# Optimization experiments

Hardware: AMD Instinct MI355X
Metric: run time of the kernel (lower is better)

The kernel has to match this reference:

```python
import jax, jax.numpy as jnp
import numpy as np

NUM_EXPERTS = 8
TOP_K = 2


def setup_inputs() -> dict:
    key = jax.random.key(0)
    ks = jax.random.split(key, 8)
    B, S, D, H, E = 4, 2048, 1024, 2048, NUM_EXPERTS
    sd = 1.0 / np.sqrt(D)
    sh = 1.0 / np.sqrt(H)
    return {
        "x": jax.random.normal(ks[0], (B, S, D), dtype=jnp.float32),
        "noise": jax.random.normal(ks[1], (B, S, E), dtype=jnp.float32),
        "router_w": jax.random.normal(ks[2], (E, D), dtype=jnp.float32) * sd,
        "router_b": jnp.zeros((E,), dtype=jnp.float32),
        "noise_w": jax.random.normal(ks[3], (E, D), dtype=jnp.float32) * sd,
        "noise_b": jnp.zeros((E,), dtype=jnp.float32),
        "w1": jax.random.normal(ks[4], (E, H, D), dtype=jnp.float32) * sd,
        "w2": jax.random.normal(ks[5], (E, D, H), dtype=jnp.float32) * sh,
        "w3": jax.random.normal(ks[6], (E, H, D), dtype=jnp.float32) * sd,
    }


def reference(x, noise, router_w, router_b, noise_w, noise_b, w1, w2, w3):
    B, S, D = x.shape
    T = B * S
    xf = x.reshape(T, D)                                  # [T, D]
    noise_f = noise.reshape(T, -1)                        # [T, E]

    # Noisy top-k router
    logits = xf @ router_w.T + router_b                   # [T, E]
    noise_logits = xf @ noise_w.T + noise_b               # [T, E]
    noisy = logits + noise_f * jax.nn.softplus(noise_logits)
    top_vals, top_idx = jax.lax.top_k(noisy, TOP_K)       # [T, K]
    sparse = jnp.full_like(noisy, -jnp.inf)
    sparse = sparse.at[jnp.arange(T)[:, None], top_idx].set(top_vals)
    gates = jax.nn.softmax(sparse, axis=-1)               # [T, E]; zero off top-k

    # Expert SwiGLU combine. Gates are exactly 0 for non-selected experts, so
    # the masked gather/scatter loop of the original equals this weighted sum.
    out = jnp.zeros_like(xf)
    for i in range(NUM_EXPERTS):
        h = jax.nn.silu(xf @ w1[i].T) * (xf @ w3[i].T)    # [T, H]
        out = out + gates[:, i:i + 1] * (h @ w2[i].T)     # [T, D]
    return out.reshape(B, S, D)
```

## Files before the change

### kernel.cpp

```cpp
#include <hip/hip_runtime.h>

typedef unsigned short u16;
typedef __attribute__((ext_vector_type(8))) __bf16 bf16x8;
typedef __attribute__((ext_vector_type(8))) short short8;
typedef __attribute__((ext_vector_type(4))) float f32x4;

#define NE 8

#define SBAR()      asm volatile("s_barrier" ::: "memory")
#define WAIT_LGKM0() do { asm volatile("s_waitcnt lgkmcnt(0)" ::: "memory"); \
                          __builtin_amdgcn_sched_barrier(0); } while (0)
#define WAIT_VM6()  asm volatile("s_waitcnt vmcnt(6)" ::: "memory")
#define WAIT_VM8()  asm volatile("s_waitcnt vmcnt(8)" ::: "memory")

__device__ __forceinline__ u16 f2bf(float f) {
    union { float f; unsigned u; } v; v.f = f;
    unsigned u = v.u;
    return (u16)((u + 0x7fffu + ((u >> 16) & 1u)) >> 16);
}

__device__ __forceinline__ f32x4 mfma16(short8 a, short8 b, f32x4 c) {
    return __builtin_amdgcn_mfma_f32_16x16x32_bf16(
        __builtin_bit_cast(bf16x8, a), __builtin_bit_cast(bf16x8, b), c, 0, 0, 0);
}

__device__ __forceinline__ void gl2lds(const u16* g, u16* l) {
    __builtin_amdgcn_global_load_lds((const __attribute__((address_space(1))) void*)g,
                                     (__attribute__((address_space(3))) void*)l,
                                     16, 0, 0);
}

__global__ void cvt_kernel(const float* __restrict__ in, u16* __restrict__ out, size_t n4) {
    size_t i = (size_t)blockIdx.x * blockDim.x + threadIdx.x;
    size_t stride = (size_t)gridDim.x * blockDim.x;
    for (; i < n4; i += stride) {
        float4 v = ((const float4*)in)[i];
        ushort4 o;
        o.x = f2bf(v.x); o.y = f2bf(v.y); o.z = f2bf(v.z); o.w = f2bf(v.w);
        ((ushort4*)out)[i] = o;
    }
}

__global__ void cvt_w13_kernel(const float* __restrict__ w1, const float* __restrict__ w3,
                               u16* __restrict__ wc, int H, int D) {
    size_t n = (size_t)NE * H * (D / 4);
    size_t i = (size_t)blockIdx.x * blockDim.x + threadIdx.x;
    size_t stride = (size_t)gridDim.x * blockDim.x;
    int d4n = D / 4;
    for (; i < n; i += stride) {
        int d4 = (int)(i % d4n);
        size_t rem = i / d4n;
        int j = (int)(rem % H);
        int e = (int)(rem / H);
        float4 v1 = ((const float4*)w1)[i];
        float4 v3 = ((const float4*)w3)[i];
        ushort4 o1, o3;
        o1.x = f2bf(v1.x); o1.y = f2bf(v1.y); o1.z = f2bf(v1.z); o1.w = f2bf(v1.w);
        o3.x = f2bf(v3.x); o3.y = f2bf(v3.y); o3.z = f2bf(v3.z); o3.w = f2bf(v3.w);
        int wcrow = ((j >> 4) << 5) + (j & 15);
        size_t o = (((size_t)e * 2 * H + wcrow) * d4n + d4);
        ((ushort4*)wc)[o] = o1;
        ((ushort4*)wc)[o + (size_t)16 * d4n] = o3;
    }
}

__global__ void router_kernel(const float* __restrict__ x, const float* __restrict__ noise,
                              const float* __restrict__ rw, const float* __restrict__ rb,
                              const float* __restrict__ nw, const float* __restrict__ nb,
                              int* __restrict__ tops, float* __restrict__ gpair,
                              u16* __restrict__ xb, int T, int D) {
    int wv = threadIdx.x >> 6;
    int lane = threadIdx.x & 63;
    int t = blockIdx.x * 4 + wv;
    if (t >= T) return;

    const float4* x4 = (const float4*)(x + (size_t)t * D) + lane * 4;
    float4 xv0 = x4[0], xv1 = x4[1], xv2 = x4[2], xv3 = x4[3];

    {
        ushort4 s0, s1, s2, s3;
        s0.x = f2bf(xv0.x); s0.y = f2bf(xv0.y); s0.z = f2bf(xv0.z); s0.w = f2bf(xv0.w);
        s1.x = f2bf(xv1.x); s1.y = f2bf(xv1.y); s1.z = f2bf(xv1.z); s1.w = f2bf(xv1.w);
        s2.x = f2bf(xv2.x); s2.y = f2bf(xv2.y); s2.z = f2bf(xv2.z); s2.w = f2bf(xv2.w);
        s3.x = f2bf(xv3.x); s3.y = f2bf(xv3.y); s3.z = f2bf(xv3.z); s3.w = f2bf(xv3.w);
        ushort4* o = (ushort4*)(xb + (size_t)t * D + lane * 16);
        o[0] = s0; o[1] = s1; o[2] = s2; o[3] = s3;
    }

    float acc[2 * NE];
#pragma unroll
    for (int e = 0; e < NE; e++) {
        const float4* w4 = (const float4*)(rw + (size_t)e * D) + lane * 4;
        float4 a = w4[0], b = w4[1], c = w4[2], d = w4[3];
        acc[e] = xv0.x*a.x + xv0.y*a.y + xv0.z*a.z + xv0.w*a.w
               + xv1.x*b.x + xv1.y*b.y + xv1.z*b.z + xv1.w*b.w
               + xv2.x*c.x + xv2.y*c.y + xv2.z*c.z + xv2.w*c.w
               + xv3.x*d.x + xv3.y*d.y + xv3.z*d.z + xv3.w*d.w;
        const float4* v4 = (const float4*)(nw + (size_t)e * D) + lane * 4;
        a = v4[0]; b = v4[1]; c = v4[2]; d = v4[3];
        acc[NE + e] = xv0.x*a.x + xv0.y*a.y + xv0.z*a.z + xv0.w*a.w
                    + xv1.x*b.x + xv1.y*b.y + xv1.z*b.z + xv1.w*b.w
                    + xv2.x*c.x + xv2.y*c.y + xv2.z*c.z + xv2.w*c.w
                    + xv3.x*d.x + xv3.y*d.y + xv3.z*d.z + xv3.w*d.w;
    }
#pragma unroll
    for (int m = 1; m < 64; m <<= 1) {
#pragma unroll
        for (int k = 0; k < 2 * NE; k++) acc[k] += __shfl_xor(acc[k], m);
    }

    if (lane == 0) {
        float v0 = -1e30f, v1 = -1e30f;
        int i0 = 0, i1 = 0;
#pragma unroll
        for (int e = 0; e < NE; e++) {
            float z = acc[NE + e] + nb[e];
            float sp = (z > 20.f) ? z : log1pf(expf(z));
            float nv = acc[e] + rb[e] + noise[(size_t)t * NE + e] * sp;
            if (nv > v0) { v1 = v0; i1 = i0; v0 = nv; i0 = e; }
            else if (nv > v1) { v1 = nv; i1 = e; }
        }
        float e1 = expf(v1 - v0);
        float inv = 1.f / (1.f + e1);
        tops[t] = i0 | (i1 << 8);
        gpair[2 * t]     = inv;
        gpair[2 * t + 1] = e1 * inv;
    }
}

__global__ void build_kernel(const int* __restrict__ tops, const float* __restrict__ gpair,
                             int* __restrict__ counts, int* __restrict__ list,
                             float* __restrict__ glist, int* __restrict__ tokslot, int T) {
    int e = blockIdx.x;
    int tid = threadIdx.x, lane = tid & 63, wv = tid >> 6;
    __shared__ int wsum[4];
    __shared__ int sbase;
    if (tid == 0) sbase = 0;
    __syncthreads();
    for (int t0 = 0; t0 < T; t0 += 256) {
        int t = t0 + tid;
        int pk = tops[t];
        int i0 = pk & 0xff, i1 = (pk >> 8) & 0xff;
        bool f0 = (i0 == e), f1 = (i1 == e);
        bool f = f0 || f1;
        unsigned long long m = __ballot(f);
        int lpos = __popcll(m & (((unsigned long long)1 << lane) - 1ull));
        if (lane == 0) wsum[wv] = __popcll(m);
        __syncthreads();
        int woff = sbase;
        for (int w = 0; w < wv; w++) woff += wsum[w];
        int tot = wsum[0] + wsum[1] + wsum[2] + wsum[3];
        if (f) {
            int pos = woff + lpos;
            list[e * T + pos]  = t;
            glist[e * T + pos] = f0 ? gpair[2 * t] : gpair[2 * t + 1];
            tokslot[2 * t + (f0 ? 0 : 1)] = (e << 16) | pos;
        }
        __syncthreads();
        if (tid == 0) sbase += tot;
    }
    __syncthreads();
    if (tid == 0) counts[e] = sbase;
}

__global__ void scan_kernel(const int* __restrict__ counts, int* __restrict__ offsets,
                            int* __restrict__ bmap, int* __restrict__ nb) {
    if (threadIdx.x == 0 && blockIdx.x == 0) {
        int s = 0, t = 0;
        for (int e = 0; e < NE; e++) {
            offsets[e] = s;
            int c = counts[e];
            s += c;
            int m = (c + 255) >> 8;
            for (int i = 0; i < m; i++) bmap[t++] = (e << 16) | i;
        }
        offsets[NE] = s;
        nb[0] = t;
    }
}


#define PH_RD_A(B, MQ) { \
    _Pragma("unroll") for (int m4 = 0; m4 < 4; m4++) { \
        aF[m4][0] = *(const short8*)&lds[B][0][(MQ)*8192 + aRow + m4*1024 + cA0]; \
        aF[m4][1] = *(const short8*)&lds[B][0][(MQ)*8192 + aRow + m4*1024 + cA1]; } }

#define PH_RD_B(B, NQ) { \
    _Pragma("unroll") for (int n2 = 0; n2 < 2; n2++) { \
        bF[n2][0] = *(const short8*)&lds[B][1][(NQ)*8192 + bRow + n2*1024 + cA0]; \
        bF[n2][1] = *(const short8*)&lds[B][1][(NQ)*8192 + bRow + n2*1024 + cA1]; } }

#define PH_MMA(MQ, NQ) do { \
    __builtin_amdgcn_s_setprio(1); \
    _Pragma("unroll") for (int m4 = 0; m4 < 4; m4++) \
        _Pragma("unroll") for (int n2 = 0; n2 < 2; n2++) { \
            acc[(MQ)*4+m4][(NQ)*2+n2] = mfma16(aF[m4][0], bF[n2][0], acc[(MQ)*4+m4][(NQ)*2+n2]); \
            acc[(MQ)*4+m4][(NQ)*2+n2] = mfma16(aF[m4][1], bF[n2][1], acc[(MQ)*4+m4][(NQ)*2+n2]); } \
    __builtin_amdgcn_s_setprio(0); } while (0)

#define STAGE(B, AB, H, p0, p1) do { \
    u16* d_ = &lds[B][AB][(H)*8192 + wid*512]; \
    gl2lds(p0, d_); gl2lds(p1, d_ + 4096); \
    p0 += 64; p1 += 64; } while (0)

#define G_TILE(B, u, nt) do { \
     \
    PH_RD_A(B, 0); PH_RD_B(B, 0); \
    if ((u) + 1 < (nt)) STAGE((B)^1, 0, 1, pA10, pA11); \
    SBAR(); WAIT_LGKM0(); \
    PH_MMA(0, 0); \
    WAIT_VM6(); \
    SBAR(); \
     \
    PH_RD_B(B, 1); \
    if ((u) + 1 < (nt)) STAGE((B)^1, 1, 1, pB10, pB11); \
    SBAR(); WAIT_LGKM0(); \
    PH_MMA(0, 1); \
    SBAR(); \
     \
    PH_RD_A(B, 1); PH_RD_B(B, 0); \
    if ((u) + 2 < (nt)) STAGE(B, 0, 0, pA00, pA01); \
    SBAR(); WAIT_LGKM0(); \
    PH_MMA(1, 0); \
    SBAR(); \
     \
    PH_RD_B(B, 1); \
    if ((u) + 2 < (nt)) STAGE(B, 1, 0, pB00, pB01); \
    SBAR(); WAIT_LGKM0(); \
    PH_MMA(1, 1); \
    WAIT_VM8(); \
    SBAR(); } while (0)

__launch_bounds__(512, 2)
__global__ void gemm1_kernel(const u16* __restrict__ xb, const u16* __restrict__ wc,
                             const int* __restrict__ counts, const int* __restrict__ offsets,
                             const int* __restrict__ list, const float* __restrict__ glist,
                             const int* __restrict__ bmap, const int* __restrict__ nb,
                             u16* __restrict__ hb, int T, int D, int H) {
    if ((int)blockIdx.y >= nb[0]) return;
    int info = bmap[blockIdx.y];
    int e = info >> 16, mblk = info & 0xffff, nblk = blockIdx.x;
    int count = counts[e];

    __shared__ u16 lds[2][2][16384];
    __shared__ int stok[256];
    __shared__ float sgate[256];

    int tid = threadIdx.x;
    int lane = tid & 63, wid = tid >> 6;

    if (tid < 256) {
        int rr = min(mblk * 256 + tid, count - 1);
        stok[tid]  = list[e * T + rr];
        sgate[tid] = glist[e * T + rr];
    }
    __syncthreads();

    const u16* wcp = wc + ((size_t)e * 2 * H + (size_t)nblk * 256) * D;

    int row_local = tid >> 3, c8 = tid & 7;
    int c_glob = c8 ^ (row_local & 7);
    const u16* pA00 = xb + (size_t)stok[row_local] * D + c_glob * 8;
    const u16* pA01 = xb + (size_t)stok[64 + row_local] * D + c_glob * 8;
    const u16* pA10 = xb + (size_t)stok[128 + row_local] * D + c_glob * 8;
    const u16* pA11 = xb + (size_t)stok[192 + row_local] * D + c_glob * 8;
    const u16* pB00 = wcp + (size_t)row_local * D + c_glob * 8;
    const u16* pB01 = wcp + (size_t)(64 + row_local) * D + c_glob * 8;
    const u16* pB10 = wcp + (size_t)(128 + row_local) * D + c_glob * 8;
    const u16* pB11 = wcp + (size_t)(192 + row_local) * D + c_glob * 8;

    int r = lane & 15, q = lane >> 4;
    int swz = r & 7;
    int cA0 = (q ^ swz) * 8;
    int cA1 = ((q + 4) ^ swz) * 8;
    int wr = wid >> 2, wc4 = wid & 3;
    int aRow = (wr * 64 + r) * 64;
    int bRow = (wc4 * 32 + r) * 64;

    f32x4 acc[8][4];
#pragma unroll
    for (int mi = 0; mi < 8; mi++)
#pragma unroll
        for (int ni = 0; ni < 4; ni++) acc[mi][ni] = (f32x4)0.f;

    short8 aF[4][2], bF[2][2];

    STAGE(0, 0, 0, pA00, pA01);
    STAGE(0, 0, 1, pA10, pA11);
    STAGE(0, 1, 0, pB00, pB01);
    STAGE(0, 1, 1, pB10, pB11);
    STAGE(1, 0, 0, pA00, pA01);
    STAGE(1, 1, 0, pB00, pB01);
    WAIT_VM6();
    SBAR();

    const int nt = D >> 6;
    for (int u = 0; u < nt; u += 2) {
        G_TILE(0, u, nt);
        G_TILE(1, u + 1, nt);
    }

    int hrow0 = offsets[e];
#pragma unroll
    for (int mi = 0; mi < 8; mi++) {
        int lrow0 = (mi >> 2) * 128 + wr * 64 + (mi & 3) * 16 + q * 4;
#pragma unroll
        for (int a = 0; a < 2; a++) {
            int col = nblk * 128 + a * 64 + wc4 * 16 + r;
#pragma unroll
            for (int tt = 0; tt < 4; tt++) {
                int lrow = lrow0 + tt;
                int grow = mblk * 256 + lrow;
                if (grow < count) {
                    float v = acc[mi][2 * a][tt];
                    float hv = v / (1.f + expf(-v)) * acc[mi][2 * a + 1][tt] * sgate[lrow];
                    hb[(size_t)(hrow0 + grow) * H + col] = f2bf(hv);
                }
            }
        }
    }
}

__launch_bounds__(512, 2)
__global__ void gemm2_kernel(const u16* __restrict__ hb, const u16* __restrict__ w2b,
                             const int* __restrict__ counts, const int* __restrict__ offsets,
                             const int* __restrict__ bmap, const int* __restrict__ nb,
                             float* __restrict__ o2, int T, int D, int H) {
    if ((int)blockIdx.y >= nb[0]) return;
    int info = bmap[blockIdx.y];
    int e = info >> 16, mblk = info & 0xffff, nblk = blockIdx.x;
    int count = counts[e];

    __shared__ u16 lds[2][2][16384];

    int tid = threadIdx.x;
    int lane = tid & 63, wid = tid >> 6;
    int off0 = offsets[e];
    const u16* w2p = w2b + ((size_t)e * D + (size_t)nblk * 256) * H;

    int row_local = tid >> 3, c8 = tid & 7;
    int c_glob = c8 ^ (row_local & 7);
    int ra00 = min(mblk * 256 + row_local, count - 1);
    int ra01 = min(mblk * 256 + 64 + row_local, count - 1);
    int ra10 = min(mblk * 256 + 128 + row_local, count - 1);
    int ra11 = min(mblk * 256 + 192 + row_local, count - 1);
    const u16* pA00 = hb + (size_t)(off0 + ra00) * H + c_glob * 8;
    const u16* pA01 = hb + (size_t)(off0 + ra01) * H + c_glob * 8;
    const u16* pA10 = hb + (size_t)(off0 + ra10) * H + c_glob * 8;
    const u16* pA11 = hb + (size_t)(off0 + ra11) * H + c_glob * 8;
    const u16* pB00 = w2p + (size_t)row_local * H + c_glob * 8;
    const u16* pB01 = w2p + (size_t)(64 + row_local) * H + c_glob * 8;
    const u16* pB10 = w2p + (size_t)(128 + row_local) * H + c_glob * 8;
    const u16* pB11 = w2p + (size_t)(192 + row_local) * H + c_glob * 8;

    int r = lane & 15, q = lane >> 4;
    int swz = r & 7;
    int cA0 = (q ^ swz) * 8;
    int cA1 = ((q + 4) ^ swz) * 8;
    int wr = wid >> 2, wc4 = wid & 3;
    int aRow = (wr * 64 + r) * 64;
    int bRow = (wc4 * 32 + r) * 64;

    f32x4 acc[8][4];
#pragma unroll
    for (int mi = 0; mi < 8; mi++)
#pragma unroll
        for (int ni = 0; ni < 4; ni++) acc[mi][ni] = (f32x4)0.f;

    short8 aF[4][2], bF[2][2];

    STAGE(0, 0, 0, pA00, pA01);
    STAGE(0, 0, 1, pA10, pA11);
    STAGE(0, 1, 0, pB00, pB01);
    STAGE(0, 1, 1, pB10, pB11);
    STAGE(1, 0, 0, pA00, pA01);
    STAGE(1, 1, 0, pB00, pB01);
    WAIT_VM6();
    SBAR();

    const int nt = H >> 6;
    for (int u = 0; u < nt; u += 2) {
        G_TILE(0, u, nt);
        G_TILE(1, u + 1, nt);
    }

#pragma unroll
    for (int mi = 0; mi < 8; mi++) {
        int lrow0 = (mi >> 2) * 128 + wr * 64 + (mi & 3) * 16 + q * 4;
#pragma unroll
        for (int tt = 0; tt < 4; tt++) {
            int grow = mblk * 256 + lrow0 + tt;
            if (grow < count) {
#pragma unroll
                for (int ni = 0; ni < 4; ni++) {
                    int col = nblk * 256 + (ni >> 1) * 128 + wc4 * 32 + (ni & 1) * 16 + r;
                    o2[(size_t)(off0 + grow) * D + col] = acc[mi][ni][tt];
                }
            }
        }
    }
}

__global__ void combine_kernel(const float* __restrict__ o2, const int* __restrict__ tokslot,
                               const int* __restrict__ offsets, float* __restrict__ out, int D) {
    int t = blockIdx.x;
    int s0 = tokslot[2 * t], s1 = tokslot[2 * t + 1];
    size_t r0 = offsets[s0 >> 16] + (s0 & 0xffff);
    size_t r1 = offsets[s1 >> 16] + (s1 & 0xffff);
    int c = threadIdx.x * 4;
    float4 a = *(const float4*)(o2 + r0 * D + c);
    float4 b = *(const float4*)(o2 + r1 * D + c);
    float4 o; o.x = a.x + b.x; o.y = a.y + b.y; o.z = a.z + b.z; o.w = a.w + b.w;
    *(float4*)(out + (size_t)t * D + c) = o;
}

extern "C" void kernel_launch(void* const* d_in, const int* in_sizes, int n_in,
                              void* d_out, int out_size, void* d_ws, size_t ws_size,
                              hipStream_t stream) {
    const float* x     = (const float*)d_in[0];
    const float* noise = (const float*)d_in[1];
    const float* rw    = (const float*)d_in[2];
    const float* rb    = (const float*)d_in[3];
    const float* nw    = (const float*)d_in[4];
    const float* nb_   = (const float*)d_in[5];
    const float* w1    = (const float*)d_in[6];
    const float* w2    = (const float*)d_in[7];
    const float* w3    = (const float*)d_in[8];
    float* out = (float*)d_out;

    const int E = NE;
    const int D = in_sizes[2] / E;
    const int T = in_sizes[0] / D;
    const int H = in_sizes[6] / (E * D);

    auto al = [](size_t v) { return (v + 255) & ~(size_t)255; };
    char* p = (char*)d_ws;
    size_t o_counts  = 0;
    size_t o_offsets = 64;
    size_t o_nb      = 128;
    size_t o_bmap    = 256;
    size_t o_tslot   = al(o_bmap  + 2048);
    size_t o_list    = al(o_tslot + (size_t)2 * T * 4);
    size_t o_glist   = al(o_list  + (size_t)E * T * 4);
    size_t o_xb      = al(o_glist + (size_t)E * T * 4);
    size_t o_wc      = al(o_xb    + (size_t)T * D * 2);
    size_t o_w2b     = al(o_wc    + (size_t)E * 2 * H * D * 2);
    size_t o_hb      = al(o_w2b   + (size_t)E * D * H * 2);

    int*   counts  = (int*)(p + o_counts);
    int*   offsets = (int*)(p + o_offsets);
    int*   nblk    = (int*)(p + o_nb);
    int*   bmap    = (int*)(p + o_bmap);
    int*   tokslot = (int*)(p + o_tslot);
    int*   list    = (int*)(p + o_list);
    float* glist   = (float*)(p + o_glist);
    u16*   xb      = (u16*)(p + o_xb);
    u16*   wc      = (u16*)(p + o_wc);
    float* o2      = (float*)(p + o_wc);
    u16*   w2b     = (u16*)(p + o_w2b);
    u16*   hb      = (u16*)(p + o_hb);
    int*   tops    = (int*)(p + o_hb);
    float* gpair   = (float*)(p + o_hb + (size_t)T * 4);

    cvt_w13_kernel<<<2048, 256, 0, stream>>>(w1, w3, wc, H, D);
    cvt_kernel<<<2048, 256, 0, stream>>>(w2, w2b, (size_t)E * D * H / 4);

    router_kernel<<<(T + 3) / 4, 256, 0, stream>>>(x, noise, rw, rb, nw, nb_,
                                                   tops, gpair, xb, T, D);
    build_kernel<<<NE, 256, 0, stream>>>(tops, gpair, counts, list, glist, tokslot, T);
    scan_kernel<<<1, 64, 0, stream>>>(counts, offsets, bmap, nblk);

    int maxb = 2 * T / 256 + NE;
    dim3 g1(2 * H / 256, maxb, 1);
    gemm1_kernel<<<g1, 512, 0, stream>>>(xb, wc, counts, offsets, list, glist,
                                         bmap, nblk, hb, T, D, H);
    dim3 g2(D / 256, maxb, 1);
    gemm2_kernel<<<g2, 512, 0, stream>>>(hb, w2b, counts, offsets,
                                         bmap, nblk, o2, T, D, H);
    combine_kernel<<<T, 256, 0, stream>>>(o2, tokslot, offsets, out, D);
}
```

Measured before the change: 625.1 us.

## Restructure GEMM main loop to hold both B fragments and reorder MFMA phases

Rewrites the shared GEMM tile macro used by both expert GEMMs. B fragments for both column halves now sit in registers, so each tile does fewer LDS read phases and barriers, and the MMA order (00, 01, 11, 10) reuses the loaded fragments. The explicit lgkmcnt waits are removed in favour of compiler-inserted ones. Global-to-LDS staging is reordered so both B halves of the next-next tile are issued together, the prologue prefetches one more stage, and the vmcnt thresholds change, with a full drain on the last tiles. This costs more registers per thread, and the changed barrier placement risks LDS races if the hazards are not fully covered.

```diff
diff --git a/kernel.cpp b/kernel.cpp
--- a/kernel.cpp
+++ b/kernel.cpp
@@ -7,11 +7,10 @@
 
 #define NE 8
 
-#define SBAR()      asm volatile("s_barrier" ::: "memory")
-#define WAIT_LGKM0() do { asm volatile("s_waitcnt lgkmcnt(0)" ::: "memory"); \
-                          __builtin_amdgcn_sched_barrier(0); } while (0)
-#define WAIT_VM6()  asm volatile("s_waitcnt vmcnt(6)" ::: "memory")
-#define WAIT_VM8()  asm volatile("s_waitcnt vmcnt(8)" ::: "memory")
+#define SBAR()   asm volatile("s_barrier" ::: "memory")
+#define WVM0()   asm volatile("s_waitcnt vmcnt(0)" ::: "memory")
+#define WVM8()   asm volatile("s_waitcnt vmcnt(8)" ::: "memory")
+#define WVM10()  asm volatile("s_waitcnt vmcnt(10)" ::: "memory")
 
 __device__ __forceinline__ u16 f2bf(float f) {
     union { float f; unsigned u; } v; v.f = f;
@@ -180,55 +179,60 @@
 }
 
 
-#define PH_RD_A(B, MQ) { \
+#define RD_A(BUF, MQ) { \
     _Pragma("unroll") for (int m4 = 0; m4 < 4; m4++) { \
-        aF[m4][0] = *(const short8*)&lds[B][0][(MQ)*8192 + aRow + m4*1024 + cA0]; \
-        aF[m4][1] = *(const short8*)&lds[B][0][(MQ)*8192 + aRow + m4*1024 + cA1]; } }
-
-#define PH_RD_B(B, NQ) { \
+        aX[m4][0] = *(const short8*)&lds[BUF][0][(MQ)*8192 + aRow + m4*1024 + cA0]; \
+        aX[m4][1] = *(const short8*)&lds[BUF][0][(MQ)*8192 + aRow + m4*1024 + cA1]; } }
+
+#define RD_B(BUF, NQ, BR) { \
     _Pragma("unroll") for (int n2 = 0; n2 < 2; n2++) { \
-        bF[n2][0] = *(const short8*)&lds[B][1][(NQ)*8192 + bRow + n2*1024 + cA0]; \
-        bF[n2][1] = *(const short8*)&lds[B][1][(NQ)*8192 + bRow + n2*1024 + cA1]; } }
-
-#define PH_MMA(MQ, NQ) do { \
+        BR[n2][0] = *(const short8*)&lds[BUF][1][(NQ)*8192 + bRow + n2*1024 + cA0]; \
+        BR[n2][1] = *(const short8*)&lds[BUF][1][(NQ)*8192 + bRow + n2*1024 + cA1]; } }
+
+#define MMA(MQ, NQ, BR) do { \
     __builtin_amdgcn_s_setprio(1); \
     _Pragma("unroll") for (int m4 = 0; m4 < 4; m4++) \
         _Pragma("unroll") for (int n2 = 0; n2 < 2; n2++) { \
-            acc[(MQ)*4+m4][(NQ)*2+n2] = mfma16(aF[m4][0], bF[n2][0], acc[(MQ)*4+m4][(NQ)*2+n2]); \
-            acc[(MQ)*4+m4][(NQ)*2+n2] = mfma16(aF[m4][1], bF[n2][1], acc[(MQ)*4+m4][(NQ)*2+n2]); } \
+            acc[(MQ)*4+m4][(NQ)*2+n2] = mfma16(aX[m4][0], BR[n2][0], acc[(MQ)*4+m4][(NQ)*2+n2]); \
+            acc[(MQ)*4+m4][(NQ)*2+n2] = mfma16(aX[m4][1], BR[n2][1], acc[(MQ)*4+m4][(NQ)*2+n2]); } \
     __builtin_amdgcn_s_setprio(0); } while (0)
 
-#define STAGE(B, AB, H, p0, p1) do { \
-    u16* d_ = &lds[B][AB][(H)*8192 + wid*512]; \
+#define STAGE(BUF, AB, HF, p0, p1) do { \
+    u16* d_ = &lds[BUF][AB][(HF)*8192 + wid*512]; \
     gl2lds(p0, d_); gl2lds(p1, d_ + 4096); \
     p0 += 64; p1 += 64; } while (0)
 
-#define G_TILE(B, u, nt) do { \
+#define TILE(BUF, t, nt) do { \
+    bool tail = (t) >= (nt) - 2; \
      \
-    PH_RD_A(B, 0); PH_RD_B(B, 0); \
-    if ((u) + 1 < (nt)) STAGE((B)^1, 0, 1, pA10, pA11); \
-    SBAR(); WAIT_LGKM0(); \
-    PH_MMA(0, 0); \
-    WAIT_VM6(); \
+    if ((t) + 1 < (nt)) STAGE(BUF ^ 1, 0, 1, pA10, pA11); \
+    RD_A(BUF, 0); RD_B(BUF, 0, bX); RD_B(BUF, 1, bY); \
+    MMA(0, 0, bX); \
     SBAR(); \
      \
-    PH_RD_B(B, 1); \
-    if ((u) + 1 < (nt)) STAGE((B)^1, 1, 1, pB10, pB11); \
-    SBAR(); WAIT_LGKM0(); \
-    PH_MMA(0, 1); \
+    if ((t) + 2 < (nt)) STAGE(BUF, 0, 0, pA00, pA01); \
+    MMA(0, 1, bY); \
+    if (tail) { WVM0(); } else { WVM10(); } \
     SBAR(); \
      \
-    PH_RD_A(B, 1); PH_RD_B(B, 0); \
-    if ((u) + 2 < (nt)) STAGE(B, 0, 0, pA00, pA01); \
-    SBAR(); WAIT_LGKM0(); \
-    PH_MMA(1, 0); \
+    if ((t) + 2 < (nt)) { STAGE(BUF, 1, 0, pB00, pB01); STAGE(BUF, 1, 1, pB10, pB11); } \
+    RD_A(BUF, 1); \
+    MMA(1, 1, bY); \
     SBAR(); \
      \
-    PH_RD_B(B, 1); \
-    if ((u) + 2 < (nt)) STAGE(B, 1, 0, pB00, pB01); \
-    SBAR(); WAIT_LGKM0(); \
-    PH_MMA(1, 1); \
-    WAIT_VM8(); \
+    MMA(1, 0, bX); \
+    if (tail) { WVM0(); } else { WVM8(); } \
+    SBAR(); } while (0)
+
+#define GEMM_PROLOGUE() do { \
+    STAGE(0, 0, 0, pA00, pA01); \
+    STAGE(0, 1, 0, pB00, pB01); \
+    STAGE(0, 1, 1, pB10, pB11); \
+    STAGE(0, 0, 1, pA10, pA11); \
+    STAGE(1, 0, 0, pA00, pA01); \
+    STAGE(1, 1, 0, pB00, pB01); \
+    STAGE(1, 1, 1, pB10, pB11); \
+    WVM8(); \
     SBAR(); } while (0)
 
 __launch_bounds__(512, 2)
@@ -283,21 +287,15 @@
 #pragma unroll
         for (int ni = 0; ni < 4; ni++) acc[mi][ni] = (f32x4)0.f;
 
-    short8 aF[4][2], bF[2][2];
-
-    STAGE(0, 0, 0, pA00, pA01);
-    STAGE(0, 0, 1, pA10, pA11);
-    STAGE(0, 1, 0, pB00, pB01);
-    STAGE(0, 1, 1, pB10, pB11);
-    STAGE(1, 0, 0, pA00, pA01);
-    STAGE(1, 1, 0, pB00, pB01);
-    WAIT_VM6();
-    SBAR();
+    short8 aX[4][2], bX[2][2], bY[2][2];
+
+    GEMM_PROLOGUE();
 
     const int nt = D >> 6;
-    for (int u = 0; u < nt; u += 2) {
-        G_TILE(0, u, nt);
-        G_TILE(1, u + 1, nt);
+#pragma unroll 1
+    for (int t = 0; t < nt; t += 2) {
+        TILE(0, t, nt);
+        TILE(1, t + 1, nt);
     }
 
     int hrow0 = offsets[e];
@@ -367,21 +365,15 @@
 #pragma unroll
         for (int ni = 0; ni < 4; ni++) acc[mi][ni] = (f32x4)0.f;
 
-    short8 aF[4][2], bF[2][2];
-
-    STAGE(0, 0, 0, pA00, pA01);
-    STAGE(0, 0, 1, pA10, pA11);
-    STAGE(0, 1, 0, pB00, pB01);
-    STAGE(0, 1, 1, pB10, pB11);
-    STAGE(1, 0, 0, pA00, pA01);
-    STAGE(1, 1, 0, pB00, pB01);
-    WAIT_VM6();
-    SBAR();
+    short8 aX[4][2], bX[2][2], bY[2][2];
+
+    GEMM_PROLOGUE();
 
     const int nt = H >> 6;
-    for (int u = 0; u < nt; u += 2) {
-        G_TILE(0, u, nt);
-        G_TILE(1, u + 1, nt);
+#pragma unroll 1
+    for (int t = 0; t < nt; t += 2) {
+        TILE(0, t, nt);
+        TILE(1, t + 1, nt);
     }
 
 #pragma unroll
```

Result: no change. 623.6 us (-0.2%).
